# Optimization experiments

Hardware: AMD Instinct MI355X
Metric: run time of the kernel (lower is better)

The kernel has to match this reference:

```python
import jax, jax.numpy as jnp
import numpy as np

CHUNK = 1024  # chunk over N to avoid materializing the full [B,N,M] distance matrix


def _min_dists(xyz1, xyz2):
    """For each point in xyz1 [B,N,3], squared L2 distance to nearest point in xyz2 [B,M,3].
    Returns [B,N]. Computed in chunks of N to bound peak memory."""
    B, N, _ = xyz1.shape
    y2 = jnp.sum(xyz2 * xyz2, axis=-1)  # [B,M]
    n_chunks = N // CHUNK
    # [n_chunks, B, CHUNK, 3]
    xc = jnp.transpose(xyz1.reshape(B, n_chunks, CHUNK, 3), (1, 0, 2, 3))

    def chunk_min(x):  # x: [B,CHUNK,3]
        x2 = jnp.sum(x * x, axis=-1)  # [B,CHUNK]
        xy = jnp.einsum('bcd,bmd->bcm', x, xyz2)  # [B,CHUNK,M]
        d = x2[:, :, None] + y2[:, None, :] - 2.0 * xy
        return jnp.min(d, axis=-1)  # [B,CHUNK]

    mins = jax.lax.map(chunk_min, xc)  # [n_chunks, B, CHUNK]
    return jnp.transpose(mins, (1, 0, 2)).reshape(B, N)


def setup_inputs() -> dict:
    key = jax.random.key(0)
    k1, k2 = jax.random.split(key)
    xyz1 = jax.random.normal(k1, (8, 8192, 3), dtype=jnp.float32)
    xyz2 = jax.random.normal(k2, (8, 8192, 3), dtype=jnp.float32)
    return {"xyz1": xyz1, "xyz2": xyz2}


def reference(xyz1, xyz2):
    # ChamferDistanceL2.forward with ignore_zeros=False and batch>1:
    # only dist1 (xyz1 -> nearest in xyz2) is used; return its mean.
    dist1 = _min_dists(xyz1, xyz2)  # [B,N]
    return jnp.mean(dist1)
```

## Files before the change

### kernel.cpp

```cpp
#include <hip/hip_runtime.h>

typedef _Float16 v8h __attribute__((ext_vector_type(8)));
typedef float v16f __attribute__((ext_vector_type(16)));

#define BB 8
#define NN 8192
#define MM 8192
#define SPLITM 8
#define CPTS 1024
#define JTC 32
#define TPB 256
#define NI 2


__device__ __forceinline__ float min3f(float a, float b, float c) {
    return fminf(fminf(a, b), c);
}

__global__ __launch_bounds__(TPB, 4) void chamfer_min_mfma(const float* __restrict__ xyz1,
                                                           const float* __restrict__ xyz2,
                                                           float* __restrict__ pmins) {
    __shared__ v8h aLds[CPTS];

    int ig     = blockIdx.x & 31;
    int jchunk = (blockIdx.x >> 5) & 7;
    int b      = blockIdx.x >> 8;
    int t = threadIdx.x;
    int wid = t >> 6;
    int lane = t & 63;
    int laneq = lane & 31;
    int half = lane >> 5;

    const float* srcA = xyz2 + ((size_t)b * MM + (size_t)jchunk * CPTS) * 3;
#pragma unroll
    for (int k = 0; k < CPTS / TPB; ++k) {
        int p = k * TPB + t;
        float x = srcA[p * 3 + 0], y = srcA[p * 3 + 1], z = srcA[p * 3 + 2];
        _Float16 h0 = (_Float16)x, h1 = (_Float16)y, h2 = (_Float16)z;
        float y0 = (float)h0, y1 = (float)h1, y2v = (float)h2;
        float s = fmaf(y0, y0, fmaf(y1, y1, y2v * y2v));
        _Float16 shi = (_Float16)s;
        _Float16 slo = (_Float16)(s - (float)shi);
        v8h v = {h0, h1, h2, shi, slo, (_Float16)1.0f, (_Float16)1.0f, (_Float16)0.0f};
        aLds[p] = v;
    }

    int it0 = (ig * 4 + wid) * NI;
    v8h bf[NI];
#pragma unroll
    for (int tt = 0; tt < NI; ++tt) {
        int i = (it0 + tt) * 32 + laneq;
        const float* p = xyz1 + ((size_t)b * NN + i) * 3;
        _Float16 h0 = (_Float16)p[0], h1 = (_Float16)p[1], h2 = (_Float16)p[2];
        float x0 = (float)h0, x1 = (float)h1, x2v = (float)h2;
        float s = fmaf(x0, x0, fmaf(x1, x1, x2v * x2v));
        _Float16 shi = (_Float16)s;
        _Float16 slo = (_Float16)(s - (float)shi);
        v8h v = {};
        if (half == 0) {
            v[0] = (_Float16)(-2.0f * x0);
            v[1] = (_Float16)(-2.0f * x1);
            v[2] = (_Float16)(-2.0f * x2v);
            v[3] = (_Float16)1.0f; v[4] = (_Float16)1.0f;
            v[5] = shi; v[6] = slo;
        }
        bf[tt] = v;
    }

    __syncthreads();

    const v16f zc = {};
    float mg[NI][4];
#pragma unroll
    for (int tt = 0; tt < NI; ++tt)
#pragma unroll
        for (int g = 0; g < 4; ++g) mg[tt][g] = 1e30f;

    int jt0 = wid * 8;
    v8h a_next = aLds[jt0 * 32 + laneq];
#pragma unroll 1
    for (int s = 0; s < JTC; ++s) {
        v8h a = a_next;
        int jn = ((s + 1) & (JTC - 1)) * 32;
        int jtn = (jn + jt0 * 32) & (CPTS - 1);
        a_next = aLds[jtn + laneq];
        v16f c[NI];
#pragma unroll
        for (int tt = 0; tt < NI; ++tt)
            c[tt] = __builtin_amdgcn_mfma_f32_32x32x16_f16(a, bf[tt], zc, 0, 0, 0);
#pragma unroll
        for (int tt = 0; tt < NI; ++tt)
#pragma unroll
            for (int g = 0; g < 4; ++g) {
                int r = 4 * g;
                mg[tt][g] = min3f(min3f(c[tt][r], c[tt][r + 1], c[tt][r + 2]),
                                  c[tt][r + 3], mg[tt][g]);
            }
    }

    float m0 = fminf(min3f(mg[0][0], mg[0][1], mg[0][2]), mg[0][3]);
    float m1 = fminf(min3f(mg[1][0], mg[1][1], mg[1][2]), mg[1][3]);
    m0 = fminf(m0, __shfl_xor(m0, 32));
    m1 = fminf(m1, __shfl_xor(m1, 32));
    int i = (it0 + half) * 32 + laneq;
    pmins[(size_t)jchunk * (BB * NN) + (size_t)b * NN + i] = half ? m1 : m0;
}

__global__ __launch_bounds__(256) void chamfer_reduce(const float* __restrict__ pmins,
                                                      float* __restrict__ out) {
    int i = blockIdx.x * 256 + threadIdx.x;
    float m = pmins[i];
#pragma unroll
    for (int sp = 1; sp < SPLITM; ++sp)
        m = fminf(m, pmins[(size_t)sp * (BB * NN) + i]);
    float s = m;
#pragma unroll
    for (int off = 32; off > 0; off >>= 1) s += __shfl_down(s, off);
    __shared__ float ls[4];
    int lane = threadIdx.x & 63, wv = threadIdx.x >> 6;
    if (lane == 0) ls[wv] = s;
    __syncthreads();
    if (threadIdx.x == 0) {
        float tt = (ls[0] + ls[1]) + (ls[2] + ls[3]);
        atomicAdd(out, tt * (1.0f / (float)(BB * NN)));
    }
}

extern "C" void kernel_launch(void* const* d_in, const int* in_sizes, int n_in,
                              void* d_out, int out_size, void* d_ws, size_t ws_size,
                              hipStream_t stream) {
    const float* xyz1 = (const float*)d_in[0];
    const float* xyz2 = (const float*)d_in[1];
    float* out = (float*)d_out;
    float* pmins = (float*)d_ws;

    hipMemsetAsync(out, 0, sizeof(float), stream);
    chamfer_min_mfma<<<BB * SPLITM * 32, TPB, 0, stream>>>(xyz1, xyz2, pmins);
    chamfer_reduce<<<(BB * NN) / 256, 256, 0, stream>>>(pmins, out);
}
```

Measured before the change: 76.10 us.

## Loop each block over four xyz2 chunks with double-buffered LDS prefetch

Cuts the M split from 8 to 2, so each block now walks 4 chunks of xyz2 in turn. It prefetches the next chunk into registers during the MFMA loop, then converts it into a second LDS buffer. The aim is to hide global-load latency, shrink the partial-min workspace, and lighten the reduce kernel. In exchange the grid has a quarter as many blocks and occupancy is lowered to 2 blocks per CU, which may weaken latency hiding. It also adds a barrier per chunk.

Measured after the change: 77.12 us. No clear change (+1.3%).

```diff
diff --git a/kernel.cpp b/kernel.cpp
--- a/kernel.cpp
+++ b/kernel.cpp
@@ -6,7 +6,8 @@
 #define BB 8
 #define NN 8192
 #define MM 8192
-#define SPLITM 8
+#define SPLITM 2
+#define NCH 4
 #define CPTS 1024
 #define JTC 32
 #define TPB 256
@@ -17,32 +18,42 @@
     return fminf(fminf(a, b), c);
 }
 
-__global__ __launch_bounds__(TPB, 4) void chamfer_min_mfma(const float* __restrict__ xyz1,
+__device__ __forceinline__ v8h cvt_a(float x, float y, float z) {
+    _Float16 h0 = (_Float16)x, h1 = (_Float16)y, h2 = (_Float16)z;
+    float y0 = (float)h0, y1 = (float)h1, y2v = (float)h2;
+    float s = fmaf(y0, y0, fmaf(y1, y1, y2v * y2v));
+    _Float16 shi = (_Float16)s;
+    _Float16 slo = (_Float16)(s - (float)shi);
+    v8h v = {h0, h1, h2, shi, slo, (_Float16)1.0f, (_Float16)1.0f, (_Float16)0.0f};
+    return v;
+}
+
+__global__ __launch_bounds__(TPB, 2) void chamfer_min_mfma(const float* __restrict__ xyz1,
                                                            const float* __restrict__ xyz2,
                                                            float* __restrict__ pmins) {
-    __shared__ v8h aLds[CPTS];
+    __shared__ v8h aLds[2][CPTS];
 
-    int ig     = blockIdx.x & 31;
-    int jchunk = (blockIdx.x >> 5) & 7;
-    int b      = blockIdx.x >> 8;
+    int ig = blockIdx.x & 31;
+    int jc = (blockIdx.x >> 5) & 1;
+    int b  = blockIdx.x >> 6;
     int t = threadIdx.x;
     int wid = t >> 6;
     int lane = t & 63;
     int laneq = lane & 31;
     int half = lane >> 5;
 
-    const float* srcA = xyz2 + ((size_t)b * MM + (size_t)jchunk * CPTS) * 3;
+    const float* srcA = xyz2 + ((size_t)b * MM + (size_t)jc * (MM / SPLITM)) * 3;
+
+    float rx[4], ry[4], rz[4];
 #pragma unroll
-    for (int k = 0; k < CPTS / TPB; ++k) {
+    for (int k = 0; k < 4; ++k) {
         int p = k * TPB + t;
-        float x = srcA[p * 3 + 0], y = srcA[p * 3 + 1], z = srcA[p * 3 + 2];
-        _Float16 h0 = (_Float16)x, h1 = (_Float16)y, h2 = (_Float16)z;
-        float y0 = (float)h0, y1 = (float)h1, y2v = (float)h2;
-        float s = fmaf(y0, y0, fmaf(y1, y1, y2v * y2v));
-        _Float16 shi = (_Float16)s;
-        _Float16 slo = (_Float16)(s - (float)shi);
-        v8h v = {h0, h1, h2, shi, slo, (_Float16)1.0f, (_Float16)1.0f, (_Float16)0.0f};
-        aLds[p] = v;
+        rx[k] = srcA[p * 3 + 0]; ry[k] = srcA[p * 3 + 1]; rz[k] = srcA[p * 3 + 2];
+    }
+#pragma unroll
+    for (int k = 0; k < 4; ++k) {
+        int p = k * TPB + t;
+        aLds[0][p] = cvt_a(rx[k], ry[k], rz[k]);
     }
 
     int it0 = (ig * 4 + wid) * NI;
@@ -76,26 +87,41 @@
 #pragma unroll
         for (int g = 0; g < 4; ++g) mg[tt][g] = 1e30f;
 
-    int jt0 = wid * 8;
-    v8h a_next = aLds[jt0 * 32 + laneq];
 #pragma unroll 1
-    for (int s = 0; s < JTC; ++s) {
-        v8h a = a_next;
-        int jn = ((s + 1) & (JTC - 1)) * 32;
-        int jtn = (jn + jt0 * 32) & (CPTS - 1);
-        a_next = aLds[jtn + laneq];
-        v16f c[NI];
+    for (int c = 0; c < NCH; ++c) {
+        int cb = c & 1;
+        if (c + 1 < NCH) {
+            const float* s2 = srcA + (size_t)(c + 1) * CPTS * 3;
 #pragma unroll
-        for (int tt = 0; tt < NI; ++tt)
-            c[tt] = __builtin_amdgcn_mfma_f32_32x32x16_f16(a, bf[tt], zc, 0, 0, 0);
+            for (int k = 0; k < 4; ++k) {
+                int p = k * TPB + t;
+                rx[k] = s2[p * 3 + 0]; ry[k] = s2[p * 3 + 1]; rz[k] = s2[p * 3 + 2];
+            }
+        }
+#pragma unroll 2
+        for (int jt = 0; jt < JTC; ++jt) {
+            v8h a = aLds[cb][jt * 32 + laneq];
+            v16f cc[NI];
 #pragma unroll
-        for (int tt = 0; tt < NI; ++tt)
+            for (int tt = 0; tt < NI; ++tt)
+                cc[tt] = __builtin_amdgcn_mfma_f32_32x32x16_f16(a, bf[tt], zc, 0, 0, 0);
 #pragma unroll
-            for (int g = 0; g < 4; ++g) {
-                int r = 4 * g;
-                mg[tt][g] = min3f(min3f(c[tt][r], c[tt][r + 1], c[tt][r + 2]),
-                                  c[tt][r + 3], mg[tt][g]);
+            for (int tt = 0; tt < NI; ++tt)
+#pragma unroll
+                for (int g = 0; g < 4; ++g) {
+                    int r = 4 * g;
+                    mg[tt][g] = min3f(min3f(cc[tt][r], cc[tt][r + 1], cc[tt][r + 2]),
+                                      cc[tt][r + 3], mg[tt][g]);
+                }
+        }
+        if (c + 1 < NCH) {
+#pragma unroll
+            for (int k = 0; k < 4; ++k) {
+                int p = k * TPB + t;
+                aLds[cb ^ 1][p] = cvt_a(rx[k], ry[k], rz[k]);
             }
+        }
+        __syncthreads();
     }
 
     float m0 = fminf(min3f(mg[0][0], mg[0][1], mg[0][2]), mg[0][3]);
@@ -103,16 +129,13 @@
     m0 = fminf(m0, __shfl_xor(m0, 32));
     m1 = fminf(m1, __shfl_xor(m1, 32));
     int i = (it0 + half) * 32 + laneq;
-    pmins[(size_t)jchunk * (BB * NN) + (size_t)b * NN + i] = half ? m1 : m0;
+    pmins[(size_t)jc * (BB * NN) + (size_t)b * NN + i] = half ? m1 : m0;
 }
 
 __global__ __launch_bounds__(256) void chamfer_reduce(const float* __restrict__ pmins,
                                                       float* __restrict__ out) {
     int i = blockIdx.x * 256 + threadIdx.x;
-    float m = pmins[i];
-#pragma unroll
-    for (int sp = 1; sp < SPLITM; ++sp)
-        m = fminf(m, pmins[(size_t)sp * (BB * NN) + i]);
+    float m = fminf(pmins[i], pmins[(size_t)(BB * NN) + i]);
     float s = m;
 #pragma unroll
     for (int off = 32; off > 0; off >>= 1) s += __shfl_down(s, off);
```
